# Performance work log

Measured on AMD Instinct MI355X. Metric: run time of the kernel, lower is better.

## Reference

```python
import jax, jax.numpy as jnp
import numpy as np


def setup_inputs() -> dict:
    key = jax.random.key(0)
    k_x, k_b = jax.random.split(key)
    B, C, H, W = 32, 512, 32, 32
    x = jax.random.normal(k_x, (B, C, H, W), dtype=jnp.float32)
    beta = jax.random.normal(k_b, (1,), dtype=jnp.float32)
    return {"x": x, "beta": beta}


def reference(x, beta):
    B, C, H, W = x.shape
    feat = x.reshape(B, C, H * W)                       # [B, C, N]
    # channel-channel Gram matrix: [B, C, C]
    attn = jnp.einsum('bcn,bdn->bcd', feat, feat)
    # DANet-style reversed scores: rowmax - score, then softmax over last dim
    attn = jnp.max(attn, axis=-1, keepdims=True) - attn
    attn = jax.nn.softmax(attn, axis=-1)
    feat_e = jnp.einsum('bcd,bdn->bcn', attn, feat).reshape(B, C, H, W)
    return beta * feat_e + x
```

## Files before the change

kernel.cpp:

```cpp
#include <hip/hip_runtime.h>
#include <math.h>

constexpr int B = 32, C = 512, N = 1024;

typedef float f32x4 __attribute__((ext_vector_type(4)));
typedef _Float16 f16x8 __attribute__((ext_vector_type(8)));
typedef unsigned short u16x4 __attribute__((ext_vector_type(4)));

__device__ __forceinline__ unsigned short f32_to_f16u(float v) {
  union { _Float16 h; unsigned short u; } cv; cv.h = (_Float16)v; return cv.u;
}
__device__ __forceinline__ float f16u_to_f32(unsigned short u) {
  union { _Float16 h; unsigned short u; } cv; cv.u = u; return (float)cv.h;
}

__device__ __forceinline__ void glds16(const void* g, void* l) {
  __builtin_amdgcn_global_load_lds((const __attribute__((address_space(1))) void*)g,
                                   (__attribute__((address_space(3))) void*)l, 16, 0, 0);
}

__global__ __launch_bounds__(256) void convert_kernel(const float* __restrict__ x,
                                                      unsigned short* __restrict__ xf,
                                                      unsigned short* __restrict__ xfT) {
  const int b = blockIdx.z;
  const int cy = blockIdx.y * 64;
  const int nx = blockIdx.x * 64;
  const int t = threadIdx.x;
  const int r = t >> 4, c4 = (t & 15) * 4;

  __shared__ unsigned T[64][65];

#pragma unroll
  for (int rr = 0; rr < 64; rr += 16) {
    const int row = rr + r;
    const size_t gi = ((size_t)b * C + cy + row) * N + nx + c4;
    const float4 v = *(const float4*)&x[gi];
    u16x4 h;
    h[0] = f32_to_f16u(v.x); h[1] = f32_to_f16u(v.y);
    h[2] = f32_to_f16u(v.z); h[3] = f32_to_f16u(v.w);
    *(u16x4*)&xf[gi] = h;
    T[row][c4 + 0] = h[0]; T[row][c4 + 1] = h[1];
    T[row][c4 + 2] = h[2]; T[row][c4 + 3] = h[3];
  }
  __syncthreads();
#pragma unroll
  for (int rr = 0; rr < 64; rr += 16) {
    const int nrow = rr + r;
    u16x4 o;
    o[0] = (unsigned short)T[c4 + 0][nrow]; o[1] = (unsigned short)T[c4 + 1][nrow];
    o[2] = (unsigned short)T[c4 + 2][nrow]; o[3] = (unsigned short)T[c4 + 3][nrow];
    *(u16x4*)&xfT[((size_t)b * N + nx + nrow) * C + cy + c4] = o;
  }
}

__global__ __launch_bounds__(1024, 4) void gram_soft_av(const unsigned short* __restrict__ xf,
                                                        const unsigned short* __restrict__ xfT,
                                                        const float* __restrict__ beta,
                                                        float* __restrict__ out) {
  const int l = blockIdx.x;
  const int xcd = l & 7, seq = l >> 3;
  const int b = xcd + 8 * (seq >> 3);
  const int i0 = (seq & 7) * 64;

  const unsigned short* __restrict__ Fh = xf  + (size_t)b * C * N;
  const unsigned short* __restrict__ FT = xfT + (size_t)b * N * C;
  float* __restrict__ ob = out + (size_t)b * C * N;

  __shared__ __align__(16) unsigned short Pb[2][512 * 32];
  __shared__ __align__(16) unsigned short Atile[64 * 512];

  const int t = threadIdx.x, wave = t >> 6, lane = t & 63;
  const int wi = wave >> 3;
  const int wj = wave & 7;
  const int lrow = lane & 15, quad = lane >> 4;
  const int srow = lane >> 2;
  const int sel  = ((lane & 3) ^ ((lane >> 3) & 3)) * 8;

  f32x4 acc[2][4] = {};

#define STAGE(k0, nb)                                                     \
  {                                                                       \
    _Pragma("unroll")                                                     \
    for (int cc = 0; cc < 2; ++cc) {                                      \
      const int chunk = wave * 2 + cc;                                    \
      const int row = chunk * 16 + srow;                                  \
      glds16(Fh + (size_t)row * N + (k0) + sel, &Pb[nb][chunk * 512]);    \
    }                                                                     \
  }

  STAGE(0, 0);

  for (int it = 0; it < 32; ++it) {
    const int k0 = it * 32;
    __syncthreads();
    if (it + 1 < 32) STAGE(k0 + 32, (it + 1) & 1);

    const unsigned short* __restrict__ Pc = Pb[it & 1];
    f16x8 ah[2], bh[4];
#pragma unroll
    for (int ti = 0; ti < 2; ++ti) {
      const int r = i0 + wi * 32 + ti * 16 + lrow;
      ah[ti] = *(const f16x8*)&Pc[r * 32 + (quad ^ ((r >> 1) & 3)) * 8];
    }
#pragma unroll
    for (int tj = 0; tj < 4; ++tj) {
      const int r = wj * 64 + tj * 16 + lrow;
      bh[tj] = *(const f16x8*)&Pc[r * 32 + (quad ^ ((r >> 1) & 3)) * 8];
    }
#pragma unroll
    for (int ti = 0; ti < 2; ++ti)
#pragma unroll
      for (int tj = 0; tj < 4; ++tj)
        acc[ti][tj] = __builtin_amdgcn_mfma_f32_16x16x32_f16(ah[ti], bh[tj], acc[ti][tj], 0, 0, 0);
  }
#undef STAGE

  __syncthreads();
  float* red = (float*)&Pb[0][0];
  float* fin = red + 512;

  float m[8];
#pragma unroll
  for (int ti = 0; ti < 2; ++ti)
#pragma unroll
    for (int rr = 0; rr < 4; ++rr)
      m[ti * 4 + rr] = fminf(fminf(acc[ti][0][rr], acc[ti][1][rr]),
                             fminf(acc[ti][2][rr], acc[ti][3][rr]));
#pragma unroll
  for (int o = 1; o < 16; o <<= 1)
#pragma unroll
    for (int s = 0; s < 8; ++s) m[s] = fminf(m[s], __shfl_xor(m[s], o, 64));
  if (lrow == 0)
#pragma unroll
    for (int ti = 0; ti < 2; ++ti)
#pragma unroll
      for (int rr = 0; rr < 4; ++rr)
        red[wave * 32 + ti * 16 + quad * 4 + rr] = m[ti * 4 + rr];
  __syncthreads();
  if (t < 64) {
    const int wig = t >> 5, loc = t & 31;
    float v = red[(wig * 8) * 32 + loc];
#pragma unroll
    for (int j = 1; j < 8; ++j) v = fminf(v, red[(wig * 8 + j) * 32 + loc]);
    fin[t] = v;
  }
  __syncthreads();

  float sm[8];
#pragma unroll
  for (int ti = 0; ti < 2; ++ti)
#pragma unroll
    for (int rr = 0; rr < 4; ++rr) {
      const float mn = fin[wi * 32 + ti * 16 + quad * 4 + rr];
      float s = 0.f;
#pragma unroll
      for (int tj = 0; tj < 4; ++tj) {
        const float e = __expf(mn - acc[ti][tj][rr]);
        acc[ti][tj][rr] = e;
        s += e;
      }
      sm[ti * 4 + rr] = s;
    }
#pragma unroll
  for (int o = 1; o < 16; o <<= 1)
#pragma unroll
    for (int s = 0; s < 8; ++s) sm[s] += __shfl_xor(sm[s], o, 64);
  if (lrow == 0)
#pragma unroll
    for (int ti = 0; ti < 2; ++ti)
#pragma unroll
      for (int rr = 0; rr < 4; ++rr)
        red[wave * 32 + ti * 16 + quad * 4 + rr] = sm[ti * 4 + rr];
  __syncthreads();
  if (t < 64) {
    const int wig = t >> 5, loc = t & 31;
    float v = 0.f;
#pragma unroll
    for (int j = 0; j < 8; ++j) v += red[(wig * 8 + j) * 32 + loc];
    fin[t] = 1.0f / v;
  }
  __syncthreads();

#pragma unroll
  for (int ti = 0; ti < 2; ++ti)
#pragma unroll
    for (int rr = 0; rr < 4; ++rr) {
      const float inv = fin[wi * 32 + ti * 16 + quad * 4 + rr];
      const int rl = wi * 32 + ti * 16 + quad * 4 + rr;
#pragma unroll
      for (int tj = 0; tj < 4; ++tj) {
        const int gcol = wj * 64 + tj * 16 + lrow;
        Atile[rl * 512 + ((((gcol >> 3) ^ (rl & 7)) << 3) | (gcol & 7))] =
            f32_to_f16u(acc[ti][tj][rr] * inv);
      }
    }
  __syncthreads();

  const float bv = beta[0];

  for (int jp = 0; jp < 2; ++jp) {
    f32x4 eacc[2][4] = {};
#define STAGE_E(k0, nb)                                                        \
    {                                                                          \
      _Pragma("unroll")                                                        \
      for (int cc = 0; cc < 2; ++cc) {                                         \
        const int chunk = wave * 2 + cc;                                       \
        const int row = chunk * 16 + srow;                                     \
        glds16(FT + (size_t)(jp * 512 + row) * C + (k0) + sel,                 \
               &Pb[nb][chunk * 512]);                                          \
      }                                                                        \
    }
    STAGE_E(0, 0);
    for (int it = 0; it < 16; ++it) {
      const int k0 = it * 32;
      __syncthreads();
      if (it + 1 < 16) STAGE_E(k0 + 32, (it + 1) & 1);

      const unsigned short* __restrict__ Pc = Pb[it & 1];
      f16x8 ah[2], bh[4];
#pragma unroll
      for (int ti = 0; ti < 2; ++ti) {
        const int ra = wi * 32 + ti * 16 + lrow;
        ah[ti] = *(const f16x8*)&Atile[ra * 512 + ((((k0 >> 3) | quad) ^ (ra & 7)) << 3)];
      }
#pragma unroll
      for (int tj = 0; tj < 4; ++tj) {
        const int rb = wj * 64 + tj * 16 + lrow;
        bh[tj] = *(const f16x8*)&Pc[rb * 32 + ((quad ^ ((rb >> 1) & 3)) << 3)];
      }
#pragma unroll
      for (int ti = 0; ti < 2; ++ti)
#pragma unroll
        for (int tj = 0; tj < 4; ++tj)
          eacc[ti][tj] = __builtin_amdgcn_mfma_f32_16x16x32_f16(ah[ti], bh[tj], eacc[ti][tj], 0, 0, 0);
    }
#undef STAGE_E

    __syncthreads();
    float* fs = (float*)&Pb[0][0] + wave * 1024;
#pragma unroll
    for (int ti = 0; ti < 2; ++ti) {
#pragma unroll
      for (int tj = 0; tj < 4; ++tj)
#pragma unroll
        for (int r = 0; r < 4; ++r)
          fs[(quad * 4 + r) * 64 + tj * 16 + lrow] = eacc[ti][tj][r];
      __syncthreads();
#pragma unroll
      for (int p = 0; p < 4; ++p) {
        const int f = p * 64 + lane;
        const int rr2 = f >> 4, cc4 = (f & 15) * 4;
        const f32x4 e = *(const f32x4*)&fs[rr2 * 64 + cc4];
        const int gr = i0 + wi * 32 + ti * 16 + rr2;
        const int gc = jp * 512 + wj * 64 + cc4;
        const size_t o = (size_t)gr * N + gc;
        const u16x4 xv = *(const u16x4*)&Fh[o];
        f32x4 ov;
        ov[0] = fmaf(bv, e[0], f16u_to_f32(xv[0]));
        ov[1] = fmaf(bv, e[1], f16u_to_f32(xv[1]));
        ov[2] = fmaf(bv, e[2], f16u_to_f32(xv[2]));
        ov[3] = fmaf(bv, e[3], f16u_to_f32(xv[3]));
        __builtin_nontemporal_store(ov, (f32x4*)&ob[o]);
      }
      __syncthreads();
    }
  }
}

extern "C" void kernel_launch(void* const* d_in, const int* in_sizes, int n_in,
                              void* d_out, int out_size, void* d_ws, size_t ws_size,
                              hipStream_t stream) {
  const float* x    = (const float*)d_in[0];
  const float* beta = (const float*)d_in[1];
  float* out = (float*)d_out;

  char* ws = (char*)d_ws;
  unsigned short* xf  = (unsigned short*)ws; ws += (size_t)B * C * N * 2;
  unsigned short* xfT = (unsigned short*)ws;

  convert_kernel<<<dim3(N / 64, C / 64, B), dim3(256),  0, stream>>>(x, xf, xfT);
  gram_soft_av  <<<dim3(256),               dim3(1024), 0, stream>>>(xf, xfT, beta, out);
}
```

Measured before the change: 181.5 us.

## Deepen Gram prefetch to four LDS stages and register-stage the AV loads

The Gram phase now keeps three async global-to-LDS loads in flight across four LDS buffers, waiting on explicit vmcnt counts before a raw barrier instead of a full __syncthreads each iteration. Atile is aliased onto the extra buffers, so total LDS stays about the same. The attention-times-value phase swaps direct-to-LDS loads for register-staged loads that are issued two iterations ahead and written to LDS after the MFMAs, with a single barrier per step. This aims to hide global latency better, but it relies on hand-tuned vmcnt values, and the register staging adds register pressure.

```diff
diff --git a/kernel.cpp b/kernel.cpp
--- a/kernel.cpp
+++ b/kernel.cpp
@@ -6,6 +6,7 @@
 typedef float f32x4 __attribute__((ext_vector_type(4)));
 typedef _Float16 f16x8 __attribute__((ext_vector_type(8)));
 typedef unsigned short u16x4 __attribute__((ext_vector_type(4)));
+typedef unsigned short u16x8 __attribute__((ext_vector_type(8)));
 
 __device__ __forceinline__ unsigned short f32_to_f16u(float v) {
   union { _Float16 h; unsigned short u; } cv; cv.h = (_Float16)v; return cv.u;
@@ -66,8 +67,8 @@
   const unsigned short* __restrict__ FT = xfT + (size_t)b * N * C;
   float* __restrict__ ob = out + (size_t)b * C * N;
 
-  __shared__ __align__(16) unsigned short Pb[2][512 * 32];
-  __shared__ __align__(16) unsigned short Atile[64 * 512];
+  __shared__ __align__(16) unsigned short Pb[4][512 * 32];
+  unsigned short* Atile = &Pb[2][0];
 
   const int t = threadIdx.x, wave = t >> 6, lane = t & 63;
   const int wi = wave >> 3;
@@ -78,7 +79,7 @@
 
   f32x4 acc[2][4] = {};
 
-#define STAGE(k0, nb)                                                     \
+#define STAGE1(k0, nb)                                                    \
   {                                                                       \
     _Pragma("unroll")                                                     \
     for (int cc = 0; cc < 2; ++cc) {                                      \
@@ -88,14 +89,19 @@
     }                                                                     \
   }
 
-  STAGE(0, 0);
+  STAGE1(0, 0);
+  STAGE1(32, 1);
+  STAGE1(64, 2);
 
   for (int it = 0; it < 32; ++it) {
     const int k0 = it * 32;
-    __syncthreads();
-    if (it + 1 < 32) STAGE(k0 + 32, (it + 1) & 1);
-
-    const unsigned short* __restrict__ Pc = Pb[it & 1];
+    if (it < 30)       asm volatile("s_waitcnt vmcnt(4)" ::: "memory");
+    else if (it == 30) asm volatile("s_waitcnt vmcnt(2)" ::: "memory");
+    else               asm volatile("s_waitcnt vmcnt(0)" ::: "memory");
+    __builtin_amdgcn_s_barrier();
+    if (it + 3 < 32) STAGE1(k0 + 96, (it + 3) & 3);
+
+    const unsigned short* __restrict__ Pc = Pb[it & 3];
     f16x8 ah[2], bh[4];
 #pragma unroll
     for (int ti = 0; ti < 2; ++ti) {
@@ -113,7 +119,7 @@
       for (int tj = 0; tj < 4; ++tj)
         acc[ti][tj] = __builtin_amdgcn_mfma_f32_16x16x32_f16(ah[ti], bh[tj], acc[ti][tj], 0, 0, 0);
   }
-#undef STAGE
+#undef STAGE1
 
   __syncthreads();
   float* red = (float*)&Pb[0][0];
@@ -200,22 +206,32 @@
 
   for (int jp = 0; jp < 2; ++jp) {
     f32x4 eacc[2][4] = {};
-#define STAGE_E(k0, nb)                                                        \
+    u16x8 rsA[2];
+#define LOADR_E(k0)                                                            \
     {                                                                          \
       _Pragma("unroll")                                                        \
       for (int cc = 0; cc < 2; ++cc) {                                         \
         const int chunk = wave * 2 + cc;                                       \
         const int row = chunk * 16 + srow;                                     \
-        glds16(FT + (size_t)(jp * 512 + row) * C + (k0) + sel,                 \
-               &Pb[nb][chunk * 512]);                                          \
+        rsA[cc] = *(const u16x8*)&FT[(size_t)(jp * 512 + row) * C + (k0) + sel]; \
       }                                                                        \
     }
-    STAGE_E(0, 0);
+#define WRITER_E(nb)                                                           \
+    {                                                                          \
+      _Pragma("unroll")                                                        \
+      for (int cc = 0; cc < 2; ++cc) {                                         \
+        const int chunk = wave * 2 + cc;                                       \
+        *(u16x8*)&Pb[nb][chunk * 512 + lane * 8] = rsA[cc];                    \
+      }                                                                        \
+    }
+    LOADR_E(0);
+    WRITER_E(0);
+    LOADR_E(32);
+    asm volatile("s_waitcnt lgkmcnt(0)" ::: "memory");
+    __builtin_amdgcn_s_barrier();
+
     for (int it = 0; it < 16; ++it) {
       const int k0 = it * 32;
-      __syncthreads();
-      if (it + 1 < 16) STAGE_E(k0 + 32, (it + 1) & 1);
-
       const unsigned short* __restrict__ Pc = Pb[it & 1];
       f16x8 ah[2], bh[4];
 #pragma unroll
@@ -233,10 +249,15 @@
 #pragma unroll
         for (int tj = 0; tj < 4; ++tj)
           eacc[ti][tj] = __builtin_amdgcn_mfma_f32_16x16x32_f16(ah[ti], bh[tj], eacc[ti][tj], 0, 0, 0);
-    }
-#undef STAGE_E
-
-    __syncthreads();
+
+      if (it + 1 < 16) WRITER_E((it + 1) & 1);
+      if (it + 2 < 16) LOADR_E(k0 + 64);
+      asm volatile("s_waitcnt lgkmcnt(0)" ::: "memory");
+      __builtin_amdgcn_s_barrier();
+    }
+#undef LOADR_E
+#undef WRITER_E
+
     float* fs = (float*)&Pb[0][0] + wave * 1024;
 #pragma unroll
     for (int ti = 0; ti < 2; ++ti) {
```

New measurement: 177.4 us. -2.2%, faster.

## Split fused attention kernel into 512 smaller blocks with A spilled to global

Applied to the files above, without the earlier changes.

Each block now handles 32 rows of the Gram matrix with 512 threads instead of 64 rows with 1024 threads, which doubles the grid to 512 blocks. The normalized attention rows are written to a global workspace and streamed back through double-buffered LDS, replacing the large shared Atile. MFMA sections get raised wave priority, and some epilogue barriers become waitcnt instructions. Together this aims to lower LDS use and raise occupancy and latency hiding. In exchange, every block re-streams the full feature matrix for its batch, so total global traffic doubles, and A now makes an extra round trip through global memory.

```diff
diff --git a/kernel.cpp b/kernel.cpp
--- a/kernel.cpp
+++ b/kernel.cpp
@@ -53,71 +53,73 @@
   }
 }
 
-__global__ __launch_bounds__(1024, 4) void gram_soft_av(const unsigned short* __restrict__ xf,
-                                                        const unsigned short* __restrict__ xfT,
-                                                        const float* __restrict__ beta,
-                                                        float* __restrict__ out) {
+__global__ __launch_bounds__(512, 4) void gram_soft_av(const unsigned short* __restrict__ xf,
+                                                       const unsigned short* __restrict__ xfT,
+                                                       unsigned short* __restrict__ Aw,
+                                                       const float* __restrict__ beta,
+                                                       float* __restrict__ out) {
   const int l = blockIdx.x;
   const int xcd = l & 7, seq = l >> 3;
-  const int b = xcd + 8 * (seq >> 3);
-  const int i0 = (seq & 7) * 64;
+  const int b = xcd + 8 * (seq >> 4);
+  const int i0 = (seq & 15) * 32;
 
   const unsigned short* __restrict__ Fh = xf  + (size_t)b * C * N;
   const unsigned short* __restrict__ FT = xfT + (size_t)b * N * C;
   float* __restrict__ ob = out + (size_t)b * C * N;
+  unsigned short* __restrict__ Ag = Aw + (size_t)b * C * C + (size_t)i0 * C;
 
   __shared__ __align__(16) unsigned short Pb[2][512 * 32];
-  __shared__ __align__(16) unsigned short Atile[64 * 512];
+  __shared__ __align__(16) unsigned short Asb[2][32 * 32];
+  __shared__ float red[256];
+  __shared__ float fin[32];
 
   const int t = threadIdx.x, wave = t >> 6, lane = t & 63;
-  const int wi = wave >> 3;
-  const int wj = wave & 7;
   const int lrow = lane & 15, quad = lane >> 4;
   const int srow = lane >> 2;
   const int sel  = ((lane & 3) ^ ((lane >> 3) & 3)) * 8;
 
   f32x4 acc[2][4] = {};
 
-#define STAGE(k0, nb)                                                     \
+#define MFMA8(AH, BH, ACC)                                                \
+  {                                                                       \
+    __builtin_amdgcn_s_setprio(1);                                        \
+    _Pragma("unroll")                                                     \
+    for (int ti = 0; ti < 2; ++ti)                                        \
+      _Pragma("unroll")                                                   \
+      for (int tj = 0; tj < 4; ++tj)                                      \
+        ACC[ti][tj] = __builtin_amdgcn_mfma_f32_16x16x32_f16(AH[ti], BH[tj], ACC[ti][tj], 0, 0, 0); \
+    __builtin_amdgcn_s_setprio(0);                                        \
+  }
+
+#define STAGE1(k0, nb)                                                    \
   {                                                                       \
     _Pragma("unroll")                                                     \
-    for (int cc = 0; cc < 2; ++cc) {                                      \
-      const int chunk = wave * 2 + cc;                                    \
+    for (int cc = 0; cc < 4; ++cc) {                                      \
+      const int chunk = wave * 4 + cc;                                    \
       const int row = chunk * 16 + srow;                                  \
       glds16(Fh + (size_t)row * N + (k0) + sel, &Pb[nb][chunk * 512]);    \
     }                                                                     \
   }
 
-  STAGE(0, 0);
-
+  STAGE1(0, 0);
   for (int it = 0; it < 32; ++it) {
-    const int k0 = it * 32;
     __syncthreads();
-    if (it + 1 < 32) STAGE(k0 + 32, (it + 1) & 1);
-
+    if (it + 1 < 32) STAGE1((it + 1) * 32, (it + 1) & 1);
     const unsigned short* __restrict__ Pc = Pb[it & 1];
     f16x8 ah[2], bh[4];
 #pragma unroll
     for (int ti = 0; ti < 2; ++ti) {
-      const int r = i0 + wi * 32 + ti * 16 + lrow;
+      const int r = i0 + ti * 16 + lrow;
       ah[ti] = *(const f16x8*)&Pc[r * 32 + (quad ^ ((r >> 1) & 3)) * 8];
     }
 #pragma unroll
     for (int tj = 0; tj < 4; ++tj) {
-      const int r = wj * 64 + tj * 16 + lrow;
+      const int r = wave * 64 + tj * 16 + lrow;
       bh[tj] = *(const f16x8*)&Pc[r * 32 + (quad ^ ((r >> 1) & 3)) * 8];
     }
-#pragma unroll
-    for (int ti = 0; ti < 2; ++ti)
-#pragma unroll
-      for (int tj = 0; tj < 4; ++tj)
-        acc[ti][tj] = __builtin_amdgcn_mfma_f32_16x16x32_f16(ah[ti], bh[tj], acc[ti][tj], 0, 0, 0);
-  }
-#undef STAGE
-
-  __syncthreads();
-  float* red = (float*)&Pb[0][0];
-  float* fin = red + 512;
+    MFMA8(ah, bh, acc);
+  }
+#undef STAGE1
 
   float m[8];
 #pragma unroll
@@ -137,11 +139,10 @@
       for (int rr = 0; rr < 4; ++rr)
         red[wave * 32 + ti * 16 + quad * 4 + rr] = m[ti * 4 + rr];
   __syncthreads();
-  if (t < 64) {
-    const int wig = t >> 5, loc = t & 31;
-    float v = red[(wig * 8) * 32 + loc];
-#pragma unroll
-    for (int j = 1; j < 8; ++j) v = fminf(v, red[(wig * 8 + j) * 32 + loc]);
+  if (t < 32) {
+    float v = red[t];
+#pragma unroll
+    for (int j = 1; j < 8; ++j) v = fminf(v, red[j * 32 + t]);
     fin[t] = v;
   }
   __syncthreads();
@@ -151,7 +152,7 @@
   for (int ti = 0; ti < 2; ++ti)
 #pragma unroll
     for (int rr = 0; rr < 4; ++rr) {
-      const float mn = fin[wi * 32 + ti * 16 + quad * 4 + rr];
+      const float mn = fin[ti * 16 + quad * 4 + rr];
       float s = 0.f;
 #pragma unroll
       for (int tj = 0; tj < 4; ++tj) {
@@ -172,11 +173,10 @@
       for (int rr = 0; rr < 4; ++rr)
         red[wave * 32 + ti * 16 + quad * 4 + rr] = sm[ti * 4 + rr];
   __syncthreads();
-  if (t < 64) {
-    const int wig = t >> 5, loc = t & 31;
+  if (t < 32) {
     float v = 0.f;
 #pragma unroll
-    for (int j = 0; j < 8; ++j) v += red[(wig * 8 + j) * 32 + loc];
+    for (int j = 0; j < 8; ++j) v += red[j * 32 + t];
     fin[t] = 1.0f / v;
   }
   __syncthreads();
@@ -185,56 +185,55 @@
   for (int ti = 0; ti < 2; ++ti)
 #pragma unroll
     for (int rr = 0; rr < 4; ++rr) {
-      const float inv = fin[wi * 32 + ti * 16 + quad * 4 + rr];
-      const int rl = wi * 32 + ti * 16 + quad * 4 + rr;
+      const float inv = fin[ti * 16 + quad * 4 + rr];
+      const int rl = ti * 16 + quad * 4 + rr;
 #pragma unroll
       for (int tj = 0; tj < 4; ++tj) {
-        const int gcol = wj * 64 + tj * 16 + lrow;
-        Atile[rl * 512 + ((((gcol >> 3) ^ (rl & 7)) << 3) | (gcol & 7))] =
-            f32_to_f16u(acc[ti][tj][rr] * inv);
-      }
-    }
+        const int gcol = wave * 64 + tj * 16 + lrow;
+        Ag[(size_t)rl * C + gcol] = f32_to_f16u(acc[ti][tj][rr] * inv);
+      }
+    }
+  asm volatile("s_waitcnt vmcnt(0)" ::: "memory");
   __syncthreads();
 
   const float bv = beta[0];
 
   for (int jp = 0; jp < 2; ++jp) {
     f32x4 eacc[2][4] = {};
-#define STAGE_E(k0, nb)                                                        \
+#define STAGE2(k0, nb)                                                         \
     {                                                                          \
       _Pragma("unroll")                                                        \
-      for (int cc = 0; cc < 2; ++cc) {                                         \
-        const int chunk = wave * 2 + cc;                                       \
+      for (int cc = 0; cc < 4; ++cc) {                                         \
+        const int chunk = wave * 4 + cc;                                       \
         const int row = chunk * 16 + srow;                                     \
         glds16(FT + (size_t)(jp * 512 + row) * C + (k0) + sel,                 \
                &Pb[nb][chunk * 512]);                                          \
       }                                                                        \
-    }
-    STAGE_E(0, 0);
-    for (int it = 0; it < 16; ++it) {
-      const int k0 = it * 32;
+      if (wave < 2)                                                            \
+        glds16(Ag + (size_t)(wave * 16 + srow) * C + (k0) + sel,               \
+               &Asb[nb][wave * 512]);                                          \
+    }
+
+    STAGE2(0, 0);
+    for (int u = 0; u < 16; ++u) {
       __syncthreads();
-      if (it + 1 < 16) STAGE_E(k0 + 32, (it + 1) & 1);
-
-      const unsigned short* __restrict__ Pc = Pb[it & 1];
+      if (u + 1 < 16) STAGE2((u + 1) * 32, (u + 1) & 1);
+      const unsigned short* __restrict__ Pc = Pb[u & 1];
+      const unsigned short* __restrict__ Ac = Asb[u & 1];
       f16x8 ah[2], bh[4];
 #pragma unroll
       for (int ti = 0; ti < 2; ++ti) {
-        const int ra = wi * 32 + ti * 16 + lrow;
-        ah[ti] = *(const f16x8*)&Atile[ra * 512 + ((((k0 >> 3) | quad) ^ (ra & 7)) << 3)];
+        const int r = ti * 16 + lrow;
+        ah[ti] = *(const f16x8*)&Ac[r * 32 + (quad ^ ((r >> 1) & 3)) * 8];
       }
 #pragma unroll
       for (int tj = 0; tj < 4; ++tj) {
-        const int rb = wj * 64 + tj * 16 + lrow;
-        bh[tj] = *(const f16x8*)&Pc[rb * 32 + ((quad ^ ((rb >> 1) & 3)) << 3)];
-      }
-#pragma unroll
-      for (int ti = 0; ti < 2; ++ti)
-#pragma unroll
-        for (int tj = 0; tj < 4; ++tj)
-          eacc[ti][tj] = __builtin_amdgcn_mfma_f32_16x16x32_f16(ah[ti], bh[tj], eacc[ti][tj], 0, 0, 0);
-    }
-#undef STAGE_E
+        const int r = wave * 64 + tj * 16 + lrow;
+        bh[tj] = *(const f16x8*)&Pc[r * 32 + (quad ^ ((r >> 1) & 3)) * 8];
+      }
+      MFMA8(ah, bh, eacc);
+    }
+#undef STAGE2
 
     __syncthreads();
     float* fs = (float*)&Pb[0][0] + wave * 1024;
@@ -245,14 +244,14 @@
 #pragma unroll
         for (int r = 0; r < 4; ++r)
           fs[(quad * 4 + r) * 64 + tj * 16 + lrow] = eacc[ti][tj][r];
-      __syncthreads();
+      asm volatile("s_waitcnt lgkmcnt(0)" ::: "memory");
 #pragma unroll
       for (int p = 0; p < 4; ++p) {
         const int f = p * 64 + lane;
         const int rr2 = f >> 4, cc4 = (f & 15) * 4;
         const f32x4 e = *(const f32x4*)&fs[rr2 * 64 + cc4];
-        const int gr = i0 + wi * 32 + ti * 16 + rr2;
-        const int gc = jp * 512 + wj * 64 + cc4;
+        const int gr = i0 + ti * 16 + rr2;
+        const int gc = jp * 512 + wave * 64 + cc4;
         const size_t o = (size_t)gr * N + gc;
         const u16x4 xv = *(const u16x4*)&Fh[o];
         f32x4 ov;
@@ -262,9 +261,10 @@
         ov[3] = fmaf(bv, e[3], f16u_to_f32(xv[3]));
         __builtin_nontemporal_store(ov, (f32x4*)&ob[o]);
       }
-      __syncthreads();
-    }
-  }
+      asm volatile("s_waitcnt lgkmcnt(0)" ::: "memory");
+    }
+  }
+#undef MFMA8
 }
 
 extern "C" void kernel_launch(void* const* d_in, const int* in_sizes, int n_in,
@@ -276,8 +276,9 @@
 
   char* ws = (char*)d_ws;
   unsigned short* xf  = (unsigned short*)ws; ws += (size_t)B * C * N * 2;
-  unsigned short* xfT = (unsigned short*)ws;
-
-  convert_kernel<<<dim3(N / 64, C / 64, B), dim3(256),  0, stream>>>(x, xf, xfT);
-  gram_soft_av  <<<dim3(256),               dim3(1024), 0, stream>>>(xf, xfT, beta, out);
-}
+  unsigned short* xfT = (unsigned short*)ws; ws += (size_t)B * N * C * 2;
+  unsigned short* Aw  = (unsigned short*)ws;
+
+  convert_kernel<<<dim3(N / 64, C / 64, B), dim3(256), 0, stream>>>(x, xf, xfT);
+  gram_soft_av  <<<dim3(512),               dim3(512), 0, stream>>>(xf, xfT, Aw, beta, out);
+}
```

Result: slower. 198.0 us (+9.1%).
